# Kernel optimization log

Measured on AMD Instinct MI355X. Metric: run time of the kernel, lower is better.

The kernel has to match this reference:

```python
import jax, jax.numpy as jnp
import numpy as np

N, E, D, H = 40000, 640000, 128, 8
HD = D // H  # per-head dim = out_dim // num_heads = 16
EPS_LN = 1e-5


def _ln(x, g, b):
    m = jnp.mean(x, axis=-1, keepdims=True)
    v = jnp.var(x, axis=-1, keepdims=True)
    return (x - m) * jax.lax.rsqrt(v + EPS_LN) * g + b


def setup_inputs() -> dict:
    key = jax.random.key(0)
    ks = jax.random.split(key, 32)
    s = 1.0 / np.sqrt(D)
    w = lambda k, shape, sc=s: jax.random.normal(k, shape, jnp.float32) * sc
    return {
        'h': w(ks[0], (N, D), 1.0),
        'e': w(ks[1], (E, D), 1.0),
        'src': jax.random.randint(ks[2], (E,), 0, N),
        'dst': jax.random.randint(ks[3], (E,), 0, N),
        'WQ': w(ks[4], (D, D)), 'WK': w(ks[5], (D, D)), 'WV': w(ks[6], (D, D)),
        'We': w(ks[7], (D, D)),
        'WOh': w(ks[8], (D, D)), 'bOh': jnp.zeros((D,), jnp.float32),
        'WOe': w(ks[9], (D, D)), 'bOe': jnp.zeros((D,), jnp.float32),
        'g1h': jnp.ones((D,), jnp.float32), 'b1h': jnp.zeros((D,), jnp.float32),
        'g1e': jnp.ones((D,), jnp.float32), 'b1e': jnp.zeros((D,), jnp.float32),
        'Wh1': w(ks[10], (D, 2 * D)), 'bh1': jnp.zeros((2 * D,), jnp.float32),
        'Wh2': w(ks[11], (2 * D, D), 1.0 / np.sqrt(2 * D)), 'bh2': jnp.zeros((D,), jnp.float32),
        'We1': w(ks[12], (D, 2 * D)), 'be1': jnp.zeros((2 * D,), jnp.float32),
        'We2': w(ks[13], (2 * D, D), 1.0 / np.sqrt(2 * D)), 'be2': jnp.zeros((D,), jnp.float32),
        'g2h': jnp.ones((D,), jnp.float32), 'b2h': jnp.zeros((D,), jnp.float32),
        'g2e': jnp.ones((D,), jnp.float32), 'b2e': jnp.zeros((D,), jnp.float32),
    }


def reference(h, e, src, dst, WQ, WK, WV, We, WOh, bOh, WOe, bOe,
              g1h, b1h, g1e, b1e, Wh1, bh1, Wh2, bh2, We1, be1, We2, be2,
              g2h, b2h, g2e, b2e):
    n = h.shape[0]
    # --- multi-head attention over graph edges ---
    Q = (h @ WQ).reshape(n, H, HD)
    K = (h @ WK).reshape(n, H, HD)
    V = (h @ WV).reshape(n, H, HD)
    pe = (e @ We).reshape(-1, H, HD)
    # per-edge elementwise score: K[src] * Q[dst] / sqrt(HD) * proj_e
    score = K[src] * Q[dst] * (1.0 / np.sqrt(HD)) * pe          # [E,H,HD]
    e_out = score.reshape(-1, D)                                 # e_out before exp
    sexp = jnp.exp(jnp.clip(jnp.sum(score, -1, keepdims=True), -5.0, 5.0))  # [E,H,1]
    wV = jax.ops.segment_sum(V[src] * sexp, dst, num_segments=n)  # [N,H,HD]
    z = jax.ops.segment_sum(sexp, dst, num_segments=n)             # [N,H,1]
    h_attn = (wV / (z + 1e-6)).reshape(n, D)
    # --- output proj + residual + LN ---
    h1 = _ln(h + h_attn @ WOh + bOh, g1h, b1h)
    e1 = _ln(e + e_out @ WOe + bOe, g1e, b1e)
    # --- FFN + residual + LN ---
    h2 = _ln(h1 + jax.nn.relu(h1 @ Wh1 + bh1) @ Wh2 + bh2, g2h, b2h)
    e2 = _ln(e1 + jax.nn.relu(e1 @ We1 + be1) @ We2 + be2, g2e, b2e)
    return (h2, e2)
```

## Files before the change

kernel.cpp:

```cpp
#include <hip/hip_runtime.h>
#include <hip/hip_bf16.h>


constexpr int N_ = 40000;
constexpr int E_ = 640000;

typedef __attribute__((ext_vector_type(8))) short bf16x8;
typedef __attribute__((ext_vector_type(4))) float f32x4;

__device__ inline short f2bf(float f) {
    union { float f; unsigned u; } v; v.f = f;
    unsigned r = v.u + 0x7FFFu + ((v.u >> 16) & 1u);
    return (short)(r >> 16);
}
__device__ inline float bf2f(unsigned short u) {
    union { unsigned u; float f; } v; v.u = ((unsigned)u) << 16; return v.f;
}
__device__ inline unsigned packbf2(float a, float b) {
    return (unsigned)(unsigned short)f2bf(a) |
           ((unsigned)(unsigned short)f2bf(b) << 16);
}

__device__ inline f32x4 mfma16(bf16x8 a, bf16x8 b, f32x4 c) {
    return __builtin_amdgcn_mfma_f32_16x16x32_bf16(a, b, c, 0, 0, 0);
}

__device__ inline float red16(float v) {
    v += __shfl_xor(v, 1);
    v += __shfl_xor(v, 2);
    v += __shfl_xor(v, 4);
    v += __shfl_xor(v, 8);
    return v;
}

template<int KSTEPS, int LDA>
__device__ inline void load_af(const short* sA, int row, int g, bf16x8* af) {
#pragma unroll
    for (int ks = 0; ks < KSTEPS; ++ks)
        af[ks] = *(const bf16x8*)(sA + row * LDA + ks * 32 + g * 8);
}

template<int KSTEPS>
__device__ inline f32x4 gemm_tileF(const bf16x8* af, const short* sW,
                                   int n, int lane, f32x4 acc) {
#pragma unroll
    for (int ks = 0; ks < KSTEPS; ++ks)
        acc = mfma16(af[ks],
                     *(const bf16x8*)(sW + ((n * 4 + ks) * 64 + lane) * 8), acc);
    return acc;
}

__device__ inline void stageWX(const short* __restrict__ Wsrc, short* sW,
                               int tid) {
    bf16x8 tmp[8];
#pragma unroll
    for (int p = 0; p < 8; ++p)
        tmp[p] = *(const bf16x8*)(Wsrc + (tid + p * 256) * 8);
#pragma unroll
    for (int p = 0; p < 8; ++p)
        *(bf16x8*)(sW + (tid + p * 256) * 8) = tmp[p];
}

__device__ inline void stage64(const float* __restrict__ gsrc, short* sA,
                               int lane, int rowB) {
    int rr = rowB + (lane >> 2);
    int c0 = (lane & 3) * 32;
    const float* gp = gsrc + (size_t)rr * 128 + c0;
    short* dp = sA + rr * 136 + c0;
#pragma unroll
    for (int p = 0; p < 4; ++p) {
        float4 x = *(const float4*)(gp + p * 8);
        float4 y = *(const float4*)(gp + p * 8 + 4);
        bf16x8 v;
        v[0] = f2bf(x.x); v[1] = f2bf(x.y); v[2] = f2bf(x.z); v[3] = f2bf(x.w);
        v[4] = f2bf(y.x); v[5] = f2bf(y.y); v[6] = f2bf(y.z); v[7] = f2bf(y.w);
        *(bf16x8*)(dp + p * 8) = v;
    }
}

__device__ inline void proj_ln(short* sA, const f32x4* eres, const short* sW,
                               const float* __restrict__ bias,
                               const float* __restrict__ gma,
                               const float* __restrict__ beta,
                               int rowB, int c, int g, int lane, f32x4* x1v) {
    bf16x8 af[4];
    load_af<4, 136>(sA, rowB + c, g, af);
    float sx[4] = {0, 0, 0, 0}, sxx[4] = {0, 0, 0, 0};
#pragma unroll
    for (int n = 0; n < 8; ++n) {
        f32x4 a = gemm_tileF<4>(af, sW, n, lane, f32x4{0.f, 0.f, 0.f, 0.f});
        const int col = n * 16 + c;
        float bo = bias[col];
#pragma unroll
        for (int r = 0; r < 4; ++r) {
            float xv = a[r] + bo + eres[n][r];
            a[r] = xv; sx[r] += xv; sxx[r] += xv * xv;
        }
        x1v[n] = a;
    }
    float mean[4], inv[4];
#pragma unroll
    for (int r = 0; r < 4; ++r) {
        float s = red16(sx[r]), s2 = red16(sxx[r]);
        mean[r] = s * 0.0078125f;
        float var = s2 * 0.0078125f - mean[r] * mean[r];
        inv[r] = rsqrtf(var + 1e-5f);
    }
#pragma unroll
    for (int n = 0; n < 8; ++n) {
        const int col = n * 16 + c;
        float gg = gma[col], bb = beta[col];
#pragma unroll
        for (int r = 0; r < 4; ++r) {
            float v1 = (x1v[n][r] - mean[r]) * inv[r] * gg + bb;
            x1v[n][r] = v1;
            sA[(rowB + g * 4 + r) * 136 + col] = f2bf(v1);
        }
    }
}

__device__ inline void ffn_lnS(short* sA, short* sW,
                               const short* __restrict__ W1t,
                               const float* __restrict__ b1,
                               const short* __restrict__ W2t,
                               const float* __restrict__ b2,
                               const float* __restrict__ gma,
                               const float* __restrict__ beta,
                               int rowB, int c, int g, int lane, int tid,
                               f32x4* x1v, float* __restrict__ outp, int tb) {
    bf16x8 af[4];
    load_af<4, 136>(sA, rowB + c, g, af);
#pragma unroll
    for (int half = 0; half < 2; ++half) {
        __syncthreads();
        stageWX(W1t + half * 16384, sW, tid);
        __syncthreads();
#pragma unroll
        for (int n2 = 0; n2 < 8; ++n2) {
            f32x4 a3 = gemm_tileF<4>(af, sW, n2, lane,
                                     f32x4{0.f, 0.f, 0.f, 0.f});
            const int col2 = half * 128 + n2 * 16 + c;
            float bb = b1[col2];
#pragma unroll
            for (int r = 0; r < 4; ++r)
                sA[(rowB + g * 4 + r) * 136 + n2 * 16 + c] =
                    f2bf(fmaxf(a3[r] + bb, 0.f));
        }
        bf16x8 a4[4];
        load_af<4, 136>(sA, rowB + c, g, a4);
        __syncthreads();
        stageWX(W2t + half * 16384, sW, tid);
        __syncthreads();
#pragma unroll
        for (int n = 0; n < 8; ++n)
            x1v[n] = gemm_tileF<4>(a4, sW, n, lane, x1v[n]);
    }
    float ty[4] = {0, 0, 0, 0}, tyy[4] = {0, 0, 0, 0};
#pragma unroll
    for (int n = 0; n < 8; ++n) {
        const int col = n * 16 + c;
        float bb = b2[col];
#pragma unroll
        for (int r = 0; r < 4; ++r) {
            float xv = x1v[n][r] + bb;
            x1v[n][r] = xv; ty[r] += xv; tyy[r] += xv * xv;
        }
    }
    float mean[4], inv[4];
#pragma unroll
    for (int r = 0; r < 4; ++r) {
        float s = red16(ty[r]), s2 = red16(tyy[r]);
        mean[r] = s * 0.0078125f;
        float var = s2 * 0.0078125f - mean[r] * mean[r];
        inv[r] = rsqrtf(var + 1e-5f);
    }
#pragma unroll
    for (int n = 0; n < 8; ++n) {
        const int col = n * 16 + c;
        float gg = gma[col], bb = beta[col];
#pragma unroll
        for (int r = 0; r < 4; ++r)
            outp[(size_t)(tb + rowB + g * 4 + r) * 128 + col] =
                (x1v[n][r] - mean[r]) * inv[r] * gg + bb;
    }
}

__global__ void prep_weights(
    const float* __restrict__ WQ, const float* __restrict__ WK,
    const float* __restrict__ WV, const float* __restrict__ We,
    const float* __restrict__ WOh, const float* __restrict__ WOe,
    const float* __restrict__ Wh1, const float* __restrict__ Wh2,
    const float* __restrict__ We1, const float* __restrict__ We2,
    short* __restrict__ out) {
    int i = blockIdx.x * 256 + threadIdx.x;
    if (i < 98304) {
        int m = i >> 14, r = i & 16383;
        const float* W = m == 0 ? WQ : m == 1 ? WK : m == 2 ? WV
                        : m == 3 ? We : m == 4 ? WOh : WOe;
        int blk = r >> 9, l = (r >> 3) & 63, j = r & 7;
        int n = blk >> 2, ks = blk & 3;
        int col = n * 16 + (l & 15);
        int k = ks * 32 + (l >> 4) * 8 + j;
        out[i] = f2bf(W[k * 128 + col]);
    } else if (i < 229376) {
        int j2 = i - 98304;
        int m = j2 >> 15, r = j2 & 32767;
        int half = r >> 14, q = r & 16383;
        int blk = q >> 9, l = (q >> 3) & 63, j = q & 7;
        int n = blk >> 2, ks = blk & 3;
        if (m == 0 || m == 2) {
            const float* W = (m == 0) ? Wh1 : We1;
            int col2 = half * 128 + n * 16 + (l & 15);
            int k = ks * 32 + (l >> 4) * 8 + j;
            out[i] = f2bf(W[k * 256 + col2]);
        } else {
            const float* W = (m == 1) ? Wh2 : We2;
            int col = n * 16 + (l & 15);
            int k = half * 128 + ks * 32 + (l >> 4) * 8 + j;
            out[i] = f2bf(W[k * 128 + col]);
        }
    }
}

__global__ void hist_kernel(const int* __restrict__ dst, int* __restrict__ cnt) {
    int i = blockIdx.x * 256 + threadIdx.x;
    if (i < E_) atomicAdd(&cnt[dst[i]], 1);
}

__global__ void __launch_bounds__(1024) scan_kernel(const int* __restrict__ cnt,
                                                    int* __restrict__ off) {
    __shared__ int part[1024];
    int t = threadIdx.x;
    int base = t * 40;
    int s = 0;
    if (base < N_) {
        int end = min(base + 40, N_);
        for (int i = base; i < end; ++i) s += cnt[i];
    }
    part[t] = s;
    __syncthreads();
    for (int d = 1; d < 1024; d <<= 1) {
        int v = (t >= d) ? part[t - d] : 0;
        __syncthreads();
        part[t] += v;
        __syncthreads();
    }
    int prefix = (t == 0) ? 0 : part[t - 1];
    if (base < N_) {
        int end = min(base + 40, N_);
        int run = prefix;
        for (int i = base; i < end; ++i) { off[i] = run; run += cnt[i]; }
    }
    if (t == 1023) off[N_] = part[1023];
}

__global__ void scatter_kernel(const int* __restrict__ src,
                               const int* __restrict__ dst,
                               const int* __restrict__ off,
                               int* __restrict__ cursor,
                               int* __restrict__ slotOf,
                               int* __restrict__ csr_src) {
    int i = blockIdx.x * 256 + threadIdx.x;
    if (i < E_) {
        int d = dst[i];
        int s = off[d] + atomicAdd(&cursor[d], 1);
        slotOf[i] = s;
        csr_src[s] = src[i];
    }
}

__global__ void __launch_bounds__(256) qkv_kernel(
    const float* __restrict__ hsrc, const short* __restrict__ Wt3,
    unsigned short* __restrict__ Qo, unsigned short* __restrict__ Ko,
    unsigned short* __restrict__ Vo) {
    __shared__ __align__(16) short sA[64 * 136];
    __shared__ __align__(16) short sW[128 * 128];
    const int tid = threadIdx.x;
    const int tb = blockIdx.x * 64;
    const int lane = tid & 63, wave = tid >> 6;
    const int c = lane & 15, g = lane >> 4;
    const int rowB = wave * 16;

    stage64(hsrc + (size_t)tb * 128, sA, lane, rowB);
    bf16x8 af[4];
    load_af<4, 136>(sA, rowB + c, g, af);

    unsigned short* outs[3] = {Qo, Ko, Vo};
#pragma unroll
    for (int w = 0; w < 3; ++w) {
        __syncthreads();
        stageWX(Wt3 + w * 16384, sW, tid);
        __syncthreads();
        unsigned short* op = outs[w];
#pragma unroll
        for (int n = 0; n < 8; ++n) {
            f32x4 a = gemm_tileF<4>(af, sW, n, lane, f32x4{0.f, 0.f, 0.f, 0.f});
            const int col = n * 16 + c;
#pragma unroll
            for (int r = 0; r < 4; ++r)
                op[(size_t)(tb + rowB + g * 4 + r) * 128 + col] =
                    (unsigned short)f2bf(a[r]);
        }
    }
}

__global__ void __launch_bounds__(256) edge_kernel(
    const float* __restrict__ e, const int* __restrict__ src,
    const int* __restrict__ dst, const int* __restrict__ slotOf,
    const unsigned short* __restrict__ Qb, const unsigned short* __restrict__ Kb,
    float* __restrict__ sexpS,
    const short* __restrict__ Wet, const short* __restrict__ WOet,
    const short* __restrict__ We1t, const short* __restrict__ We2t,
    const float* __restrict__ bOe,
    const float* __restrict__ g1e, const float* __restrict__ b1e,
    const float* __restrict__ be1, const float* __restrict__ be2,
    const float* __restrict__ g2e, const float* __restrict__ b2e,
    float* __restrict__ e2out) {
    __shared__ __align__(16) short sA[64 * 136];
    __shared__ __align__(16) short sW[128 * 128];
    const int tid = threadIdx.x;
    const int tb = blockIdx.x * 64;
    const int lane = tid & 63, wave = tid >> 6;
    const int c = lane & 15, g = lane >> 4;
    const int rowB = wave * 16;

    stageWX(Wet, sW, tid);
    stage64(e + (size_t)tb * 128, sA, lane, rowB);

    int pre = 0;
    {
        int li = lane & 15;
        if (lane < 16)       pre = src[tb + rowB + li];
        else if (lane < 32)  pre = dst[tb + rowB + li];
        else if (lane < 48)  pre = slotOf[tb + rowB + li];
    }

    f32x4 eres[8];
#pragma unroll
    for (int n = 0; n < 8; ++n)
#pragma unroll
        for (int r = 0; r < 4; ++r)
            eres[n][r] = e[(size_t)(tb + rowB + g * 4 + r) * 128 + n * 16 + c];

    __syncthreads();

    bf16x8 af[4];
    load_af<4, 136>(sA, rowB + c, g, af);
#pragma unroll
    for (int n = 0; n < 8; ++n) {
        f32x4 p = gemm_tileF<4>(af, sW, n, lane, f32x4{0.f, 0.f, 0.f, 0.f});
#pragma unroll
        for (int r = 0; r < 4; ++r)
            sA[(rowB + g * 4 + r) * 136 + n * 16 + c] = f2bf(p[r]);
    }

    const int head = lane >> 3;
#pragma unroll
    for (int b = 0; b < 2; ++b) {
        unsigned kreg[8], qreg[8];
#pragma unroll
        for (int k = 0; k < 8; ++k) {
            int sI = __shfl(pre, b * 8 + k);
            kreg[k] = *(const unsigned*)(Kb + (size_t)sI * 128 + 2 * lane);
        }
#pragma unroll
        for (int k = 0; k < 8; ++k) {
            int dI = __shfl(pre, 16 + b * 8 + k);
            qreg[k] = *(const unsigned*)(Qb + (size_t)dI * 128 + 2 * lane);
        }
#pragma unroll
        for (int k = 0; k < 8; ++k) {
            const int i = b * 8 + k;
            const int row = rowB + i;
            const int slot = __shfl(pre, 32 + i);
            unsigned pp = *(const unsigned*)(sA + row * 136 + 2 * lane);
            float sc0 = bf2f((unsigned short)kreg[k]) *
                        bf2f((unsigned short)qreg[k]) * 0.25f *
                        bf2f((unsigned short)pp);
            float sc1 = bf2f((unsigned short)(kreg[k] >> 16)) *
                        bf2f((unsigned short)(qreg[k] >> 16)) * 0.25f *
                        bf2f((unsigned short)(pp >> 16));
            *(unsigned*)(sA + row * 136 + 2 * lane) = packbf2(sc0, sc1);
            float s = sc0 + sc1;
            s += __shfl_xor(s, 1);
            s += __shfl_xor(s, 2);
            s += __shfl_xor(s, 4);
            s = fminf(5.f, fmaxf(-5.f, s));
            if ((lane & 7) == 0)
                sexpS[(size_t)slot * 8 + head] = __expf(s);
        }
    }

    __syncthreads();
    stageWX(WOet, sW, tid);
    __syncthreads();

    f32x4 x1v[8];
    proj_ln(sA, eres, sW, bOe, g1e, b1e, rowB, c, g, lane, x1v);
    ffn_lnS(sA, sW, We1t, be1, We2t, be2, g2e, b2e,
            rowB, c, g, lane, tid, x1v, e2out, tb);
}

__global__ void __launch_bounds__(256) node_kernel(
    const float* __restrict__ h, const unsigned short* __restrict__ Vb,
    const float* __restrict__ sexpS,
    const int* __restrict__ off, const int* __restrict__ csr_src,
    const short* __restrict__ WOht, const short* __restrict__ Wh1t,
    const short* __restrict__ Wh2t,
    const float* __restrict__ bOh,
    const float* __restrict__ g1h, const float* __restrict__ b1h,
    const float* __restrict__ bh1, const float* __restrict__ bh2,
    const float* __restrict__ g2h, const float* __restrict__ b2h,
    float* __restrict__ h2out) {
    __shared__ __align__(16) short sA[64 * 136];
    __shared__ __align__(16) short sW[128 * 128];
    const int tid = threadIdx.x;
    const int tb = blockIdx.x * 64;
    const int lane = tid & 63, wave = tid >> 6;
    const int c = lane & 15, g = lane >> 4;
    const int rowB = wave * 16;
    const int head = lane >> 3;

    stageWX(WOht, sW, tid);

    f32x4 hres[8];
#pragma unroll
    for (int n = 0; n < 8; ++n)
#pragma unroll
        for (int r = 0; r < 4; ++r)
            hres[n][r] = h[(size_t)(tb + rowB + g * 4 + r) * 128 + n * 16 + c];

    int offv = (lane < 17) ? off[tb + rowB + lane] : 0;

    for (int i = 0; i < 16; ++i) {
        const int b0 = __shfl(offv, i), b1 = __shfl(offv, i + 1);
        float a0 = 0.f, a1 = 0.f, zz = 0.f;
        for (int j0 = b0; j0 < b1; j0 += 8) {
            int jj = j0 + (lane & 7);
            int ci = (jj < b1) ? csr_src[jj] : 0;
            unsigned vv[8]; float sv[8];
#pragma unroll
            for (int k = 0; k < 8; ++k) {
                bool ok = (j0 + k) < b1;
                int cs = __shfl(ci, k);
                vv[k] = ok ? *(const unsigned*)(Vb + (size_t)cs * 128 + 2 * lane)
                           : 0u;
                sv[k] = ok ? sexpS[(size_t)(j0 + k) * 8 + head] : 0.f;
            }
#pragma unroll
            for (int k = 0; k < 8; ++k) {
                a0 += bf2f((unsigned short)vv[k]) * sv[k];
                a1 += bf2f((unsigned short)(vv[k] >> 16)) * sv[k];
                zz += sv[k];
            }
        }
        float iz = 1.f / (zz + 1e-6f);
        *(unsigned*)(sA + (rowB + i) * 136 + 2 * lane) = packbf2(a0 * iz, a1 * iz);
    }

    __syncthreads();

    f32x4 x1v[8];
    proj_ln(sA, hres, sW, bOh, g1h, b1h, rowB, c, g, lane, x1v);
    ffn_lnS(sA, sW, Wh1t, bh1, Wh2t, bh2, g2h, b2h,
            rowB, c, g, lane, tid, x1v, h2out, tb);
}

extern "C" void kernel_launch(void* const* d_in, const int* in_sizes, int n_in,
                              void* d_out, int out_size, void* d_ws,
                              size_t ws_size, hipStream_t stream) {
    const float* h   = (const float*)d_in[0];
    const float* e   = (const float*)d_in[1];
    const int*   src = (const int*)d_in[2];
    const int*   dst = (const int*)d_in[3];
    const float* WQ  = (const float*)d_in[4];
    const float* WK  = (const float*)d_in[5];
    const float* WV  = (const float*)d_in[6];
    const float* We  = (const float*)d_in[7];
    const float* WOh = (const float*)d_in[8];
    const float* bOh = (const float*)d_in[9];
    const float* WOe = (const float*)d_in[10];
    const float* bOe = (const float*)d_in[11];
    const float* g1h = (const float*)d_in[12];
    const float* b1h = (const float*)d_in[13];
    const float* g1e = (const float*)d_in[14];
    const float* b1e = (const float*)d_in[15];
    const float* Wh1 = (const float*)d_in[16];
    const float* bh1 = (const float*)d_in[17];
    const float* Wh2 = (const float*)d_in[18];
    const float* bh2 = (const float*)d_in[19];
    const float* We1 = (const float*)d_in[20];
    const float* be1 = (const float*)d_in[21];
    const float* We2 = (const float*)d_in[22];
    const float* be2 = (const float*)d_in[23];
    const float* g2h = (const float*)d_in[24];
    const float* b2h = (const float*)d_in[25];
    const float* g2e = (const float*)d_in[26];
    const float* b2e = (const float*)d_in[27];

    unsigned short* Qb = (unsigned short*)d_ws;
    unsigned short* Kb = Qb + (size_t)N_ * 128;
    unsigned short* Vb = Kb + (size_t)N_ * 128;
    float* sexpS = (float*)(Vb + (size_t)N_ * 128);
    int* cnt     = (int*)(sexpS + (size_t)E_ * 8);
    int* cursor  = cnt + N_;
    int* off     = cursor + N_;
    int* slotOf  = off + N_ + 16;
    int* csr_src = slotOf + E_;
    short* Wb    = (short*)(csr_src + E_);

    float* h2out = (float*)d_out;
    float* e2out = h2out + (size_t)N_ * 128;

    prep_weights<<<896, 256, 0, stream>>>(WQ, WK, WV, We, WOh, WOe,
                                          Wh1, Wh2, We1, We2, Wb);
    hipMemsetAsync(cnt, 0, 2 * N_ * sizeof(int), stream);
    hist_kernel<<<E_ / 256, 256, 0, stream>>>(dst, cnt);
    scan_kernel<<<1, 1024, 0, stream>>>(cnt, off);
    scatter_kernel<<<E_ / 256, 256, 0, stream>>>(src, dst, off, cursor,
                                                 slotOf, csr_src);
    qkv_kernel<<<N_ / 64, 256, 0, stream>>>(h, Wb, Qb, Kb, Vb);
    edge_kernel<<<E_ / 64, 256, 0, stream>>>(
        e, src, dst, slotOf, Qb, Kb, sexpS,
        Wb + 3 * 16384, Wb + 5 * 16384,
        Wb + 98304 + 2 * 32768, Wb + 98304 + 3 * 32768,
        bOe, g1e, b1e, be1, be2, g2e, b2e, e2out);
    node_kernel<<<N_ / 64, 256, 0, stream>>>(
        h, Vb, sexpS, off, csr_src,
        Wb + 4 * 16384, Wb + 98304, Wb + 98304 + 32768,
        bOh, g1h, b1h, bh1, bh2, g2h, b2h, h2out);
}
```

Before: 530.3 us.

## Process 128 edges per block with 512 threads to amortize weight staging

The edge kernel now handles 128 edge rows per block with 8 waves instead of 64 rows with 4 waves. Each staged weight matrix in shared memory is reused by twice as many rows, and staging work is split across 512 threads. The bf16 conversion also switches to the HIP intrinsic. In exchange the block uses more LDS (sA doubles), so fewer blocks may fit per CU, and block-wide syncs now wait on more waves.

```diff
diff --git a/kernel.cpp b/kernel.cpp
--- a/kernel.cpp
+++ b/kernel.cpp
@@ -9,9 +9,9 @@
 typedef __attribute__((ext_vector_type(4))) float f32x4;
 
 __device__ inline short f2bf(float f) {
-    union { float f; unsigned u; } v; v.f = f;
-    unsigned r = v.u + 0x7FFFu + ((v.u >> 16) & 1u);
-    return (short)(r >> 16);
+    union { __hip_bfloat16 b; short s; } u;
+    u.b = __float2bfloat16(f);
+    return u.s;
 }
 __device__ inline float bf2f(unsigned short u) {
     union { unsigned u; float f; } v; v.u = ((unsigned)u) << 16; return v.f;
@@ -50,15 +50,17 @@
     return acc;
 }
 
+template<int NT>
 __device__ inline void stageWX(const short* __restrict__ Wsrc, short* sW,
                                int tid) {
-    bf16x8 tmp[8];
-#pragma unroll
-    for (int p = 0; p < 8; ++p)
-        tmp[p] = *(const bf16x8*)(Wsrc + (tid + p * 256) * 8);
-#pragma unroll
-    for (int p = 0; p < 8; ++p)
-        *(bf16x8*)(sW + (tid + p * 256) * 8) = tmp[p];
+    constexpr int P = 2048 / NT;
+    bf16x8 tmp[P];
+#pragma unroll
+    for (int p = 0; p < P; ++p)
+        tmp[p] = *(const bf16x8*)(Wsrc + (tid + p * NT) * 8);
+#pragma unroll
+    for (int p = 0; p < P; ++p)
+        *(bf16x8*)(sW + (tid + p * NT) * 8) = tmp[p];
 }
 
 __device__ inline void stage64(const float* __restrict__ gsrc, short* sA,
@@ -119,6 +121,7 @@
     }
 }
 
+template<int NT>
 __device__ inline void ffn_lnS(short* sA, short* sW,
                                const short* __restrict__ W1t,
                                const float* __restrict__ b1,
@@ -133,7 +136,7 @@
 #pragma unroll
     for (int half = 0; half < 2; ++half) {
         __syncthreads();
-        stageWX(W1t + half * 16384, sW, tid);
+        stageWX<NT>(W1t + half * 16384, sW, tid);
         __syncthreads();
 #pragma unroll
         for (int n2 = 0; n2 < 8; ++n2) {
@@ -149,7 +152,7 @@
         bf16x8 a4[4];
         load_af<4, 136>(sA, rowB + c, g, a4);
         __syncthreads();
-        stageWX(W2t + half * 16384, sW, tid);
+        stageWX<NT>(W2t + half * 16384, sW, tid);
         __syncthreads();
 #pragma unroll
         for (int n = 0; n < 8; ++n)
@@ -289,7 +292,7 @@
 #pragma unroll
     for (int w = 0; w < 3; ++w) {
         __syncthreads();
-        stageWX(Wt3 + w * 16384, sW, tid);
+        stageWX<256>(Wt3 + w * 16384, sW, tid);
         __syncthreads();
         unsigned short* op = outs[w];
 #pragma unroll
@@ -304,7 +307,7 @@
     }
 }
 
-__global__ void __launch_bounds__(256) edge_kernel(
+__global__ void __launch_bounds__(512) edge_kernel(
     const float* __restrict__ e, const int* __restrict__ src,
     const int* __restrict__ dst, const int* __restrict__ slotOf,
     const unsigned short* __restrict__ Qb, const unsigned short* __restrict__ Kb,
@@ -316,15 +319,15 @@
     const float* __restrict__ be1, const float* __restrict__ be2,
     const float* __restrict__ g2e, const float* __restrict__ b2e,
     float* __restrict__ e2out) {
-    __shared__ __align__(16) short sA[64 * 136];
+    __shared__ __align__(16) short sA[128 * 136];
     __shared__ __align__(16) short sW[128 * 128];
     const int tid = threadIdx.x;
-    const int tb = blockIdx.x * 64;
+    const int tb = blockIdx.x * 128;
     const int lane = tid & 63, wave = tid >> 6;
     const int c = lane & 15, g = lane >> 4;
     const int rowB = wave * 16;
 
-    stageWX(Wet, sW, tid);
+    stageWX<512>(Wet, sW, tid);
     stage64(e + (size_t)tb * 128, sA, lane, rowB);
 
     int pre = 0;
@@ -392,13 +395,13 @@
     }
 
     __syncthreads();
-    stageWX(WOet, sW, tid);
+    stageWX<512>(WOet, sW, tid);
     __syncthreads();
 
     f32x4 x1v[8];
     proj_ln(sA, eres, sW, bOe, g1e, b1e, rowB, c, g, lane, x1v);
-    ffn_lnS(sA, sW, We1t, be1, We2t, be2, g2e, b2e,
-            rowB, c, g, lane, tid, x1v, e2out, tb);
+    ffn_lnS<512>(sA, sW, We1t, be1, We2t, be2, g2e, b2e,
+                 rowB, c, g, lane, tid, x1v, e2out, tb);
 }
 
 __global__ void __launch_bounds__(256) node_kernel(
@@ -421,7 +424,7 @@
     const int rowB = wave * 16;
     const int head = lane >> 3;
 
-    stageWX(WOht, sW, tid);
+    stageWX<256>(WOht, sW, tid);
 
     f32x4 hres[8];
 #pragma unroll
@@ -462,8 +465,8 @@
 
     f32x4 x1v[8];
     proj_ln(sA, hres, sW, bOh, g1h, b1h, rowB, c, g, lane, x1v);
-    ffn_lnS(sA, sW, Wh1t, bh1, Wh2t, bh2, g2h, b2h,
-            rowB, c, g, lane, tid, x1v, h2out, tb);
+    ffn_lnS<256>(sA, sW, Wh1t, bh1, Wh2t, bh2, g2h, b2h,
+                 rowB, c, g, lane, tid, x1v, h2out, tb);
 }
 
 extern "C" void kernel_launch(void* const* d_in, const int* in_sizes, int n_in,
@@ -520,7 +523,7 @@
     scatter_kernel<<<E_ / 256, 256, 0, stream>>>(src, dst, off, cursor,
                                                  slotOf, csr_src);
     qkv_kernel<<<N_ / 64, 256, 0, stream>>>(h, Wb, Qb, Kb, Vb);
-    edge_kernel<<<E_ / 64, 256, 0, stream>>>(
+    edge_kernel<<<E_ / 128, 512, 0, stream>>>(
         e, src, dst, slotOf, Qb, Kb, sexpS,
         Wb + 3 * 16384, Wb + 5 * 16384,
         Wb + 98304 + 2 * 32768, Wb + 98304 + 3 * 32768,
```

Measured after the change: 497.5 us. 6.2% less time.
